# Performance work log

Hardware: AMD Instinct MI355X
Metric: run time of the kernel (lower is better)

The kernel has to match this reference:

```python
import jax, jax.numpy as jnp
import numpy as np

B, S, D = 2, 2048, 1024
E, K, F = 64, 6, 1408
DFF = 4096
N = B * S
CAP = 768
Z_LOSS_W = 1e-6
MOE_SCALE = 0.5  # 1/(1 + (num_shared_experts > 0))


def setup_inputs() -> dict:
    key = jax.random.key(0)
    ks = jax.random.split(key, 7)
    x = jax.random.normal(ks[0], (B, S, D), jnp.float32)
    router_w = jax.random.normal(ks[1], (E, D), jnp.float32) * 0.01
    experts_w12 = jax.random.normal(ks[2], (E, D, 2 * F), jnp.float32) * 0.011
    experts_w3 = jax.random.normal(ks[3], (E, F, D), jnp.float32) * 0.011
    gate_w = jax.random.normal(ks[4], (DFF, D), jnp.float32) * 0.011
    up_w = jax.random.normal(ks[5], (DFF, D), jnp.float32) * 0.011
    down_w = jax.random.normal(ks[6], (D, DFF), jnp.float32) * 0.011
    return {"x": x, "router_w": router_w, "experts_w12": experts_w12,
            "experts_w3": experts_w3, "gate_w": gate_w, "up_w": up_w,
            "down_w": down_w}


def reference(x, router_w, experts_w12, experts_w3, gate_w, up_w, down_w):
    b, s, d = x.shape
    h = x.reshape(-1, d)                    # [N, D]
    n = h.shape[0]

    # ---- router (fp32) ----
    logits = h @ router_w.T                 # [N, E]
    scores = jax.nn.sigmoid(logits)
    z_loss = jnp.mean(logits ** 2) * Z_LOSS_W
    # expert_bias defaults to zeros -> selection on scores directly
    _, topk_idx = jax.lax.top_k(scores, K)  # [N, K]
    topk_idx = jnp.clip(topk_idx, 0, E - 1)
    topk_logits = jnp.take_along_axis(logits, topk_idx, axis=1)
    gating = jax.nn.softmax(topk_logits, axis=-1).astype(jnp.bfloat16)  # [N, K]

    # ---- shared expert (dense SwiGLU) ----
    shared = (jax.nn.silu(h @ gate_w.T) * (h @ up_w.T)) @ down_w.T  # [N, D]

    # ---- dispatch: sort token-expert pairs by expert, scatter into padded buffer ----
    flat_idx = topk_idx.reshape(-1)                     # [N*K]
    order = jnp.argsort(flat_idx)
    expert_sorted = flat_idx[order]                     # [N*K]
    token_ids = jnp.repeat(jnp.arange(n), K)[order]     # source token per pair
    counts = jnp.bincount(flat_idx, length=E)
    starts = jnp.concatenate([jnp.zeros((1,), counts.dtype), jnp.cumsum(counts)[:-1]])
    intra = jnp.arange(n * K) - starts[expert_sorted]   # slot within expert
    valid = intra < CAP
    dest = jnp.where(valid, expert_sorted * CAP + intra, E * CAP)  # overflow -> trash row

    grouped = h[token_ids]                              # [N*K, D]
    padded = jnp.zeros((E * CAP + 1, d), h.dtype).at[dest].set(grouped)
    padded = padded[:-1].reshape(E, CAP, d)             # [E, CAP, D]

    # ---- per-expert grouped GEMM (SwiGLU) ----
    h12 = jnp.einsum('ecd,edf->ecf', padded, experts_w12)   # [E, CAP, 2F]
    h1, h2 = jnp.split(h12, 2, axis=-1)
    act = jax.nn.silu(h1) * h2
    eout = jnp.einsum('ecf,efd->ecd', act, experts_w3)      # [E, CAP, D]

    # ---- combine: gather back and scatter-add into token order ----
    eout_flat = jnp.concatenate([eout.reshape(-1, d), jnp.zeros((1, d), eout.dtype)])
    full = eout_flat[dest]                              # [N*K, D]
    g_sorted = gating.reshape(-1)[order].astype(h.dtype)
    weighted = full * g_sorted[:, None]
    routed = jnp.zeros((n, d), h.dtype).at[token_ids].add(weighted)

    # eval mode: aux_loss = 0, route_scale = 1.0
    out = (shared + routed) * MOE_SCALE
    return out.reshape(b, s, d), z_loss
```

## Files before the change

### kernel.cpp

```cpp
#include <hip/hip_runtime.h>
#include <stdint.h>
#include <math.h>

#define NTOK 4096
#define DIM  1024
#define NEXP 64
#define KSEL 6
#define FF   1408
#define FF2  2816
#define DFFC 4096
#define CAPE 768

typedef __bf16 bf16x8 __attribute__((ext_vector_type(8)));
typedef float  f32x4  __attribute__((ext_vector_type(4)));

__device__ __forceinline__ float bf2f(uint32_t h) {
  union { uint32_t u; float f; } v; v.u = h << 16; return v.f;
}
__device__ __forceinline__ uint16_t f2bf(float f) {
  union { float f; uint32_t u; } v; v.f = f;
  return (uint16_t)((v.u + 0x7fffu + ((v.u >> 16) & 1u)) >> 16);
}
__device__ __forceinline__ uint32_t pk_bf16(float a, float b) {
  uint32_t r;
  asm("v_cvt_pk_bf16_f32 %0, %1, %2" : "=v"(r) : "v"(a), "v"(b));
  return r;
}
__device__ __forceinline__ int swzh(int r) { return ((r ^ (r >> 2)) & 7) << 3; }

__device__ __forceinline__ void load_lds16(const void* g, void* l) {
  __builtin_amdgcn_global_load_lds((const __attribute__((address_space(1))) void*)g,
                                   (__attribute__((address_space(3))) void*)l, 16, 0, 0);
}

__global__ __launch_bounds__(256) void router_kernel(const float* __restrict__ x,
                                                     const float* __restrict__ rw,
                                                     int* __restrict__ topk,
                                                     uint16_t* __restrict__ gating,
                                                     float* __restrict__ tokz,
                                                     uint16_t* __restrict__ hb) {
  __shared__ float hs[16 * DIM];
  __shared__ float lg[16][NEXP];
  const int tid = threadIdx.x;
  const int t0 = blockIdx.x * 16;
  const float4* xin = (const float4*)(x + (size_t)t0 * DIM);
  float4* hs4 = (float4*)hs;
  for (int i = tid; i < 16 * DIM / 4; i += 256) hs4[i] = xin[i];
  __syncthreads();
  {
    ushort4* hbo = (ushort4*)(hb + (size_t)t0 * DIM);
    for (int i = tid; i < 16 * DIM / 4; i += 256) {
      float4 v = hs4[i];
      ushort4 o;
      o.x = f2bf(v.x); o.y = f2bf(v.y); o.z = f2bf(v.z); o.w = f2bf(v.w);
      hbo[i] = o;
    }
  }
  const int e = tid >> 2, q = tid & 3;
  float part[16];
#pragma unroll
  for (int tt = 0; tt < 16; tt++) part[tt] = 0.f;
  const float4* rw4 = (const float4*)(rw + (size_t)e * DIM + q * 256);
  for (int i = 0; i < 64; i++) {
    float4 w = rw4[i];
#pragma unroll
    for (int tt = 0; tt < 16; tt++) {
      float4 h = *(const float4*)(hs + tt * DIM + q * 256 + i * 4);
      part[tt] += h.x * w.x + h.y * w.y + h.z * w.z + h.w * w.w;
    }
  }
#pragma unroll
  for (int tt = 0; tt < 16; tt++) {
    float v = part[tt];
    v += __shfl_xor(v, 1);
    v += __shfl_xor(v, 2);
    if (q == 0) lg[tt][e] = v;
  }
  __syncthreads();
  const int wid = tid >> 6, lane = tid & 63;
  for (int ti = 0; ti < 4; ti++) {
    int tt = wid * 4 + ti;
    float v = lg[tt][lane];
    float z = v * v;
#pragma unroll
    for (int off = 32; off; off >>= 1) z += __shfl_xor(z, off);
    float bv[KSEL]; int bi[KSEL];
#pragma unroll
    for (int s = 0; s < KSEL; s++) {
      float m = v; int mi = lane;
#pragma unroll
      for (int off = 32; off; off >>= 1) {
        float om = __shfl_xor(m, off); int oi = __shfl_xor(mi, off);
        if (om > m || (om == m && oi < mi)) { m = om; mi = oi; }
      }
      bv[s] = m; bi[s] = mi;
      if (lane == mi) v = -3.0e38f;
    }
    if (lane == 0) {
      int t = t0 + tt;
      tokz[t] = z;
      float mx = bv[0];
      float ex[KSEL], sum = 0.f;
#pragma unroll
      for (int s = 0; s < KSEL; s++) { ex[s] = expf(bv[s] - mx); sum += ex[s]; }
      float inv = 1.f / sum;
#pragma unroll
      for (int s = 0; s < KSEL; s++) {
        topk[t * KSEL + s] = bi[s];
        gating[t * KSEL + s] = f2bf(ex[s] * inv);
      }
    }
  }
}

__global__ __launch_bounds__(256) void zred_kernel(const float* __restrict__ tz,
                                                   float* __restrict__ out) {
  __shared__ float s[256];
  float a = 0.f;
  for (int i = threadIdx.x; i < NTOK; i += 256) a += tz[i];
  s[threadIdx.x] = a; __syncthreads();
  for (int st = 128; st; st >>= 1) {
    if (threadIdx.x < (unsigned)st) s[threadIdx.x] += s[threadIdx.x + st];
    __syncthreads();
  }
  if (threadIdx.x == 0) out[0] = s[0] * (1e-6f / ((float)NTOK * (float)NEXP));
}

__global__ __launch_bounds__(64) void dispatch_kernel(const int* __restrict__ topk,
                                                      int* __restrict__ dest,
                                                      int* __restrict__ invmap,
                                                      int* __restrict__ counts) {
  const int e = blockIdx.x;
  const int lane = threadIdx.x;
  int base = 0;
  for (int it = 0; it < (NTOK * KSEL) / 64; it++) {
    int p = it * 64 + lane;
    int ex = topk[p];
    bool m = (ex == e);
    unsigned long long mask = __ballot(m);
    if (m) {
      int intra = base + __popcll(mask & ((1ull << lane) - 1ull));
      if (intra < CAPE) {
        dest[p] = e * CAPE + intra;
        invmap[e * CAPE + intra] = p / KSEL;
      } else {
        dest[p] = -1;
      }
    }
    base += __popcll(mask);
  }
  if (lane == 0) counts[e] = base < CAPE ? base : CAPE;
}

#define BM 128
#define BN 128
#define BKK 64

template<int EPI, int BSRC, bool IND, bool REMAP>
__global__ __launch_bounds__(256, 3) void gemm_f(const uint16_t* __restrict__ A,
                                                 const float* __restrict__ B,
                                                 const float* __restrict__ B2,
                                                 void* __restrict__ C,
                                                 const int* __restrict__ invmap,
                                                 const int* __restrict__ counts,
                                                 int K, int lda, int ldb, int ldc,
                                                 long long strideA, long long strideB,
                                                 long long strideC, int grouped,
                                                 int nM, int nN) {
  const int per = gridDim.x >> 3;
  const int w = ((int)blockIdx.x & 7) * per + ((int)blockIdx.x >> 3);
  const int mi = w % nM;
  const int q1 = w / nM;
  const int ni = q1 % nN;
  const int e  = q1 / nN;
  int cnt = 1 << 30;
  if (grouped) {
    cnt = counts[e];
    if (mi * BM >= cnt) return;
  }
  const int bm0 = mi * BM, bn0 = ni * BN;
  const uint16_t* Ab = A + (size_t)e * strideA;
  const float* Bb = B + (size_t)e * strideB;
  __shared__ alignas(16) uint16_t sA[2][BM * BKK];
  __shared__ alignas(16) uint16_t sB[BN * BKK];
  const int tid = threadIdx.x, wid = tid >> 6, lane = tid & 63;

  const int sa = tid >> 3;
  const int colk = (((tid & 7) ^ ((sa ^ (sa >> 2)) & 7)) * 8);
  const uint16_t* ap[4];
#pragma unroll
  for (int i = 0; i < 4; i++) {
    int row = i * 32 + sa;
    int ar = bm0 + row;
    if constexpr (IND) {
      int cr = ar < cnt ? ar : (cnt - 1);
      ar = invmap[e * CAPE + cr];
    }
    ap[i] = Ab + (size_t)ar * lda + colk;
  }

  const float* bpa = nullptr;
  const float* bpb = nullptr;
  if constexpr (BSRC == 1) {
    const int kc = (tid & 15) * 4;
    bpa = Bb + (size_t)(bn0 + (tid >> 4)) * ldb + kc;
  } else if constexpr (BSRC == 3) {
    const int kc = (tid & 15) * 4;
    const int gcol = (bn0 >> 1) + (tid >> 4);
    bpa = B  + (size_t)gcol * ldb + kc;
    bpb = B2 + (size_t)gcol * ldb + kc;
  } else {
    const int n0 = 4 * (tid & 31);
    int vn0 = bn0 + n0;
    int ng0;
    if constexpr (REMAP) {
      int blk = vn0 >> 5, lo = vn0 & 31;
      ng0 = blk * 16 + (lo & 15) + (lo < 16 ? 0 : FF);
    } else {
      ng0 = vn0;
    }
    bpa = Bb + (size_t)(4 * (tid >> 5)) * ldb + ng0;
  }

  auto loadB = [&](f32x4 (&v)[8]) {
    if constexpr (BSRC == 1) {
#pragma unroll
      for (int it = 0; it < 8; it++)
        v[it] = *(const f32x4*)(bpa + (size_t)(it * 16) * ldb);
      bpa += BKK;
    } else if constexpr (BSRC == 3) {
#pragma unroll
      for (int it = 0; it < 8; it++) {
        const float* s = (it & 1) ? bpb : bpa;
        v[it] = *(const f32x4*)(s + (size_t)((it >> 1) * 16) * ldb);
      }
      bpa += BKK; bpb += BKK;
    } else {
#pragma unroll
      for (int i2 = 0; i2 < 2; i2++)
#pragma unroll
        for (int j = 0; j < 4; j++)
          v[i2 * 4 + j] = *(const f32x4*)(bpa + (size_t)(32 * i2 + j) * ldb);
      bpa += (size_t)BKK * ldb;
    }
  };
  auto issueA = [&](int buf) {
#pragma unroll
    for (int i = 0; i < 4; i++) {
      load_lds16(ap[i], sA[buf] + i * 2048 + wid * 512);
      ap[i] += BKK;
    }
  };
  auto writeB = [&](f32x4 (&v)[8]) {
    if constexpr (BSRC == 1 || BSRC == 3) {
      const int kc = (tid & 15) * 4;
#pragma unroll
      for (int it = 0; it < 8; it++) {
        int nr = (tid >> 4) + it * 16;
        uint2 p;
        p.x = pk_bf16(v[it][0], v[it][1]);
        p.y = pk_bf16(v[it][2], v[it][3]);
        *(uint2*)(sB + nr * BKK + (kc ^ swzh(nr))) = p;
      }
    } else {
      const int n0 = 4 * (tid & 31);
#pragma unroll
      for (int i2 = 0; i2 < 2; i2++) {
        int kk0 = 4 * (tid >> 5) + 32 * i2;
#pragma unroll
        for (int c = 0; c < 4; c++) {
          int nr = n0 + c;
          uint2 p;
          p.x = pk_bf16(v[i2 * 4 + 0][c], v[i2 * 4 + 1][c]);
          p.y = pk_bf16(v[i2 * 4 + 2][c], v[i2 * 4 + 3][c]);
          *(uint2*)(sB + nr * BKK + (kk0 ^ swzh(nr))) = p;
        }
      }
    }
  };

  f32x4 zero = {0.f, 0.f, 0.f, 0.f};
  f32x4 acc[4][4];
#pragma unroll
  for (int i = 0; i < 4; i++)
#pragma unroll
    for (int j = 0; j < 4; j++) acc[i][j] = zero;
  const int wm = wid >> 1, wn = wid & 1;

  f32x4 bv[8];
  issueA(0);
  loadB(bv);

  const int T = K / BKK;
  for (int t = 0; t < T; t++) {
    const int cur = t & 1, nb = cur ^ 1;
    const bool more = (t + 1 < T);
    if (more) issueA(nb);
    writeB(bv);
    if (more) loadB(bv);
    asm volatile("s_waitcnt lgkmcnt(0)" ::: "memory");
    __builtin_amdgcn_sched_barrier(0);
    __builtin_amdgcn_s_barrier();
    __builtin_amdgcn_sched_barrier(0);
#pragma unroll
    for (int ks = 0; ks < 2; ks++) {
      const int kb = ks * 32 + (lane >> 4) * 8;
      bf16x8 af[4], bfr[4];
#pragma unroll
      for (int f = 0; f < 4; f++) {
        int rowA = wm * 64 + f * 16 + (lane & 15);
        af[f] = *(const bf16x8*)(sA[cur] + rowA * BKK + (kb ^ swzh(rowA)));
      }
#pragma unroll
      for (int f = 0; f < 4; f++) {
        int rowB = wn * 64 + f * 16 + (lane & 15);
        bfr[f] = *(const bf16x8*)(sB + rowB * BKK + (kb ^ swzh(rowB)));
      }
#pragma unroll
      for (int fm = 0; fm < 4; fm++)
#pragma unroll
        for (int fn = 0; fn < 4; fn++)
          acc[fm][fn] = __builtin_amdgcn_mfma_f32_16x16x32_bf16(af[fm], bfr[fn],
                                                                acc[fm][fn], 0, 0, 0);
    }
    __builtin_amdgcn_sched_barrier(0);
    __builtin_amdgcn_s_barrier();
    __builtin_amdgcn_sched_barrier(0);
  }

  const int lr = (lane >> 4) * 4, lc = lane & 15;
  if constexpr (EPI == 2) {
    uint16_t* outp = (uint16_t*)C + (size_t)e * strideC;
#pragma unroll
    for (int fm = 0; fm < 4; fm++) {
#pragma unroll
      for (int fp = 0; fp < 2; fp++) {
        f32x4 g = acc[fm][2 * fp], u = acc[fm][2 * fp + 1];
        int fcol = (bn0 >> 1) + wn * 32 + fp * 16 + lc;
#pragma unroll
        for (int j = 0; j < 4; j++) {
          int r = bm0 + wm * 64 + fm * 16 + lr + j;
          float gv = g[j];
          float sv = (gv / (1.f + expf(-gv))) * u[j];
          outp[(size_t)r * ldc + fcol] = f2bf(sv);
        }
      }
    }
  } else if constexpr (EPI == 1) {
    float* outp = (float*)C + (size_t)e * strideC;
#pragma unroll
    for (int fm = 0; fm < 4; fm++)
#pragma unroll
      for (int fn = 0; fn < 4; fn++) {
        int col = bn0 + wn * 64 + fn * 16 + lc;
#pragma unroll
        for (int j = 0; j < 4; j++) {
          int r = bm0 + wm * 64 + fm * 16 + lr + j;
          outp[(size_t)r * ldc + col] = acc[fm][fn][j];
        }
      }
  } else {
    uint16_t* outp = (uint16_t*)C + (size_t)e * strideC;
#pragma unroll
    for (int fm = 0; fm < 4; fm++)
#pragma unroll
      for (int fn = 0; fn < 4; fn++) {
        int col = bn0 + wn * 64 + fn * 16 + lc;
#pragma unroll
        for (int j = 0; j < 4; j++) {
          int r = bm0 + wm * 64 + fm * 16 + lr + j;
          outp[(size_t)r * ldc + col] = f2bf(acc[fm][fn][j]);
        }
      }
  }
}

__global__ __launch_bounds__(256) void combine_kernel(const float* __restrict__ shout,
                                                      const uint16_t* __restrict__ eout,
                                                      const int* __restrict__ dest,
                                                      const uint16_t* __restrict__ gating,
                                                      float* __restrict__ out) {
  const int t = blockIdx.x;
  const int d0 = threadIdx.x * 4;
  float4 sh = *(const float4*)(shout + (size_t)t * DIM + d0);
  float rx = 0.f, ry = 0.f, rz = 0.f, rw = 0.f;
#pragma unroll
  for (int k = 0; k < KSEL; k++) {
    int dp = dest[t * KSEL + k];
    if (dp >= 0) {
      float gw = bf2f(gating[t * KSEL + k]);
      ushort4 ev = *(const ushort4*)(eout + (size_t)dp * DIM + d0);
      rx += gw * bf2f(ev.x);
      ry += gw * bf2f(ev.y);
      rz += gw * bf2f(ev.z);
      rw += gw * bf2f(ev.w);
    }
  }
  float4 o;
  o.x = (sh.x + rx) * 0.5f;
  o.y = (sh.y + ry) * 0.5f;
  o.z = (sh.z + rz) * 0.5f;
  o.w = (sh.w + rw) * 0.5f;
  *(float4*)(out + (size_t)t * DIM + d0) = o;
}

extern "C" void kernel_launch(void* const* d_in, const int* in_sizes, int n_in,
                              void* d_out, int out_size, void* d_ws, size_t ws_size,
                              hipStream_t stream) {
  (void)in_sizes; (void)n_in; (void)out_size; (void)ws_size;
  const float* x   = (const float*)d_in[0];
  const float* rw  = (const float*)d_in[1];
  const float* w12 = (const float*)d_in[2];
  const float* w3  = (const float*)d_in[3];
  const float* gw  = (const float*)d_in[4];
  const float* uw  = (const float*)d_in[5];
  const float* dw  = (const float*)d_in[6];
  float* out = (float*)d_out;

  char* ws = (char*)d_ws;
  size_t off = 0;
  auto alloc = [&](size_t sz) -> void* {
    void* p = ws + off;
    off += (sz + 255) & ~(size_t)255;
    return p;
  };
  uint16_t* HB    = (uint16_t*)alloc((size_t)NTOK * DIM * 2);
  uint16_t* S1    = (uint16_t*)alloc((size_t)NTOK * DFFC * 2);
  uint16_t* ACT   = (uint16_t*)alloc((size_t)NEXP * CAPE * FF * 2);
  uint16_t* EOUT  = (uint16_t*)alloc((size_t)NEXP * CAPE * DIM * 2);
  float* SHOUT    = (float*)alloc((size_t)NTOK * DIM * 4);
  int* TOPKB      = (int*)alloc((size_t)NTOK * KSEL * 4);
  uint16_t* GATING= (uint16_t*)alloc((size_t)NTOK * KSEL * 2);
  int* DEST       = (int*)alloc((size_t)NTOK * KSEL * 4);
  int* INVMAP     = (int*)alloc((size_t)NEXP * CAPE * 4);
  int* COUNTS     = (int*)alloc((size_t)NEXP * 4);
  float* TOKZ     = (float*)alloc((size_t)NTOK * 4);

  router_kernel<<<NTOK / 16, 256, 0, stream>>>(x, rw, TOPKB, GATING, TOKZ, HB);
  dispatch_kernel<<<NEXP, 64, 0, stream>>>(TOPKB, DEST, INVMAP, COUNTS);
  zred_kernel<<<1, 256, 0, stream>>>(TOKZ, out + (size_t)NTOK * DIM);

  gemm_f<2, 3, false, false><<<(NTOK / BM) * (2 * DFFC / BN), 256, 0, stream>>>(
      HB, gw, uw, S1, nullptr, nullptr, DIM, DIM, DIM, DFFC, 0, 0, 0, 0,
      NTOK / BM, 2 * DFFC / BN);
  gemm_f<1, 1, false, false><<<(NTOK / BM) * (DIM / BN), 256, 0, stream>>>(
      S1, dw, nullptr, SHOUT, nullptr, nullptr, DFFC, DFFC, DFFC, DIM, 0, 0, 0, 0,
      NTOK / BM, DIM / BN);

  gemm_f<2, 2, true, true><<<(CAPE / BM) * (FF2 / BN) * NEXP, 256, 0, stream>>>(
      HB, w12, nullptr, ACT, INVMAP, COUNTS, DIM, DIM, FF2, FF,
      0, (long long)DIM * FF2, (long long)CAPE * FF, 1, CAPE / BM, FF2 / BN);
  gemm_f<0, 2, false, false><<<(CAPE / BM) * (DIM / BN) * NEXP, 256, 0, stream>>>(
      ACT, w3, nullptr, EOUT, nullptr, COUNTS, FF, FF, DIM, DIM,
      (long long)CAPE * FF, (long long)FF * DIM, (long long)CAPE * DIM, 1,
      CAPE / BM, DIM / BN);

  combine_kernel<<<NTOK, 256, 0, stream>>>(SHOUT, EOUT, DEST, GATING, out);
}
```

Measured before the change: 773.6 us.

## Widen GEMM tile to 128x256 with two B half-loads per step

Measured after the change: 1.414 ms. 1.83x slower.

```diff
diff --git a/kernel.cpp b/kernel.cpp
--- a/kernel.cpp
+++ b/kernel.cpp
@@ -153,11 +153,11 @@
 }
 
 #define BM 128
-#define BN 128
+#define BN 256
 #define BKK 64
 
 template<int EPI, int BSRC, bool IND, bool REMAP>
-__global__ __launch_bounds__(256, 3) void gemm_f(const uint16_t* __restrict__ A,
+__global__ __launch_bounds__(256, 2) void gemm_f(const uint16_t* __restrict__ A,
                                                  const float* __restrict__ B,
                                                  const float* __restrict__ B2,
                                                  void* __restrict__ C,
@@ -199,50 +199,64 @@
     ap[i] = Ab + (size_t)ar * lda + colk;
   }
 
-  const float* bpa = nullptr;
-  const float* bpb = nullptr;
+  const float* bpa[2] = {nullptr, nullptr};
+  const float* bpb[2] = {nullptr, nullptr};
   if constexpr (BSRC == 1) {
     const int kc = (tid & 15) * 4;
-    bpa = Bb + (size_t)(bn0 + (tid >> 4)) * ldb + kc;
+#pragma unroll
+    for (int h = 0; h < 2; h++)
+      bpa[h] = Bb + (size_t)(bn0 + h * 128 + (tid >> 4)) * ldb + kc;
   } else if constexpr (BSRC == 3) {
     const int kc = (tid & 15) * 4;
-    const int gcol = (bn0 >> 1) + (tid >> 4);
-    bpa = B  + (size_t)gcol * ldb + kc;
-    bpb = B2 + (size_t)gcol * ldb + kc;
+#pragma unroll
+    for (int h = 0; h < 2; h++) {
+      const int gcol = ((bn0 + h * 128) >> 1) + (tid >> 4);
+      bpa[h] = B  + (size_t)gcol * ldb + kc;
+      bpb[h] = B2 + (size_t)gcol * ldb + kc;
+    }
   } else {
-    const int n0 = 4 * (tid & 31);
-    int vn0 = bn0 + n0;
-    int ng0;
-    if constexpr (REMAP) {
-      int blk = vn0 >> 5, lo = vn0 & 31;
-      ng0 = blk * 16 + (lo & 15) + (lo < 16 ? 0 : FF);
+#pragma unroll
+    for (int h = 0; h < 2; h++) {
+      int vn0 = bn0 + h * 128 + 4 * (tid & 31);
+      int ng0;
+      if constexpr (REMAP) {
+        int blk = vn0 >> 5, lo = vn0 & 31;
+        ng0 = blk * 16 + (lo & 15) + (lo < 16 ? 0 : FF);
+      } else {
+        ng0 = vn0;
+      }
+      bpa[h] = Bb + (size_t)(4 * (tid >> 5)) * ldb + ng0;
+    }
+  }
+
+  auto loadB = [&](int h, f32x4 (&v)[8]) {
+    if constexpr (BSRC == 1) {
+#pragma unroll
+      for (int it = 0; it < 8; it++)
+        v[it] = *(const f32x4*)(bpa[h] + (size_t)(it * 16) * ldb);
+      bpa[h] += BKK;
+    } else if constexpr (BSRC == 3) {
+#pragma unroll
+      for (int it = 0; it < 8; it++) {
+        const float* s = (it & 1) ? bpb[h] : bpa[h];
+        v[it] = *(const f32x4*)(s + (size_t)((it >> 1) * 16) * ldb);
+      }
+      bpa[h] += BKK; bpb[h] += BKK;
     } else {
-      ng0 = vn0;
-    }
-    bpa = Bb + (size_t)(4 * (tid >> 5)) * ldb + ng0;
-  }
-
-  auto loadB = [&](f32x4 (&v)[8]) {
-    if constexpr (BSRC == 1) {
-#pragma unroll
-      for (int it = 0; it < 8; it++)
-        v[it] = *(const f32x4*)(bpa + (size_t)(it * 16) * ldb);
-      bpa += BKK;
-    } else if constexpr (BSRC == 3) {
-#pragma unroll
-      for (int it = 0; it < 8; it++) {
-        const float* s = (it & 1) ? bpb : bpa;
-        v[it] = *(const f32x4*)(s + (size_t)((it >> 1) * 16) * ldb);
-      }
-      bpa += BKK; bpb += BKK;
-    } else {
 #pragma unroll
       for (int i2 = 0; i2 < 2; i2++)
 #pragma unroll
         for (int j = 0; j < 4; j++)
-          v[i2 * 4 + j] = *(const f32x4*)(bpa + (size_t)(32 * i2 + j) * ldb);
-      bpa += (size_t)BKK * ldb;
-    }
+          v[i2 * 4 + j] = *(const f32x4*)(bpa[h] + (size_t)(4 * (tid >> 5) + 32 * i2 + j - 4 * (tid >> 5)) * ldb + (size_t)(4 * (tid >> 5)) * 0);
+    }
+  };
+  auto loadB2 = [&](int h, f32x4 (&v)[8]) {
+#pragma unroll
+    for (int i2 = 0; i2 < 2; i2++)
+#pragma unroll
+      for (int j = 0; j < 4; j++)
+        v[i2 * 4 + j] = *(const f32x4*)(bpa[h] + (size_t)(32 * i2 + j) * ldb);
+    bpa[h] += (size_t)BKK * ldb;
   };
   auto issueA = [&](int buf) {
 #pragma unroll
@@ -251,19 +265,19 @@
       ap[i] += BKK;
     }
   };
-  auto writeB = [&](f32x4 (&v)[8]) {
+  auto writeB = [&](int h, f32x4 (&v)[8]) {
     if constexpr (BSRC == 1 || BSRC == 3) {
       const int kc = (tid & 15) * 4;
 #pragma unroll
       for (int it = 0; it < 8; it++) {
-        int nr = (tid >> 4) + it * 16;
+        int nr = h * 128 + (tid >> 4) + it * 16;
         uint2 p;
         p.x = pk_bf16(v[it][0], v[it][1]);
         p.y = pk_bf16(v[it][2], v[it][3]);
         *(uint2*)(sB + nr * BKK + (kc ^ swzh(nr))) = p;
       }
     } else {
-      const int n0 = 4 * (tid & 31);
+      const int n0 = h * 128 + 4 * (tid & 31);
 #pragma unroll
       for (int i2 = 0; i2 < 2; i2++) {
         int kk0 = 4 * (tid >> 5) + 32 * i2;
@@ -278,26 +292,32 @@
       }
     }
   };
+  auto loadBh = [&](int h, f32x4 (&v)[8]) {
+    if constexpr (BSRC == 2) loadB2(h, v); else loadB(h, v);
+  };
 
   f32x4 zero = {0.f, 0.f, 0.f, 0.f};
-  f32x4 acc[4][4];
+  f32x4 acc[4][8];
 #pragma unroll
   for (int i = 0; i < 4; i++)
 #pragma unroll
-    for (int j = 0; j < 4; j++) acc[i][j] = zero;
+    for (int j = 0; j < 8; j++) acc[i][j] = zero;
   const int wm = wid >> 1, wn = wid & 1;
 
-  f32x4 bv[8];
+  f32x4 bv0[8], bv1[8];
   issueA(0);
-  loadB(bv);
+  loadBh(0, bv0);
+  loadBh(1, bv1);
 
   const int T = K / BKK;
   for (int t = 0; t < T; t++) {
     const int cur = t & 1, nb = cur ^ 1;
     const bool more = (t + 1 < T);
     if (more) issueA(nb);
-    writeB(bv);
-    if (more) loadB(bv);
+    writeB(0, bv0);
+    if (more) loadBh(0, bv0);
+    writeB(1, bv1);
+    if (more) loadBh(1, bv1);
     asm volatile("s_waitcnt lgkmcnt(0)" ::: "memory");
     __builtin_amdgcn_sched_barrier(0);
     __builtin_amdgcn_s_barrier();
@@ -305,21 +325,21 @@
 #pragma unroll
     for (int ks = 0; ks < 2; ks++) {
       const int kb = ks * 32 + (lane >> 4) * 8;
-      bf16x8 af[4], bfr[4];
+      bf16x8 af[4], bfr[8];
 #pragma unroll
       for (int f = 0; f < 4; f++) {
         int rowA = wm * 64 + f * 16 + (lane & 15);
         af[f] = *(const bf16x8*)(sA[cur] + rowA * BKK + (kb ^ swzh(rowA)));
       }
 #pragma unroll
-      for (int f = 0; f < 4; f++) {
-        int rowB = wn * 64 + f * 16 + (lane & 15);
+      for (int f = 0; f < 8; f++) {
+        int rowB = wn * 128 + f * 16 + (lane & 15);
         bfr[f] = *(const bf16x8*)(sB + rowB * BKK + (kb ^ swzh(rowB)));
       }
 #pragma unroll
       for (int fm = 0; fm < 4; fm++)
 #pragma unroll
-        for (int fn = 0; fn < 4; fn++)
+        for (int fn = 0; fn < 8; fn++)
           acc[fm][fn] = __builtin_amdgcn_mfma_f32_16x16x32_bf16(af[fm], bfr[fn],
                                                                 acc[fm][fn], 0, 0, 0);
     }
@@ -334,9 +354,9 @@
 #pragma unroll
     for (int fm = 0; fm < 4; fm++) {
 #pragma unroll
-      for (int fp = 0; fp < 2; fp++) {
+      for (int fp = 0; fp < 4; fp++) {
         f32x4 g = acc[fm][2 * fp], u = acc[fm][2 * fp + 1];
-        int fcol = (bn0 >> 1) + wn * 32 + fp * 16 + lc;
+        int fcol = (bn0 >> 1) + wn * 64 + fp * 16 + lc;
 #pragma unroll
         for (int j = 0; j < 4; j++) {
           int r = bm0 + wm * 64 + fm * 16 + lr + j;
@@ -351,8 +371,8 @@
 #pragma unroll
     for (int fm = 0; fm < 4; fm++)
 #pragma unroll
-      for (int fn = 0; fn < 4; fn++) {
-        int col = bn0 + wn * 64 + fn * 16 + lc;
+      for (int fn = 0; fn < 8; fn++) {
+        int col = bn0 + wn * 128 + fn * 16 + lc;
 #pragma unroll
         for (int j = 0; j < 4; j++) {
           int r = bm0 + wm * 64 + fm * 16 + lr + j;
@@ -364,8 +384,8 @@
 #pragma unroll
     for (int fm = 0; fm < 4; fm++)
 #pragma unroll
-      for (int fn = 0; fn < 4; fn++) {
-        int col = bn0 + wn * 64 + fn * 16 + lc;
+      for (int fn = 0; fn < 8; fn++) {
+        int col = bn0 + wn * 128 + fn * 16 + lc;
 #pragma unroll
         for (int j = 0; j < 4; j++) {
           int r = bm0 + wm * 64 + fm * 16 + lr + j;
```
